# Kernel tuning notes

Hardware: AMD Instinct MI355X
Metric: run time of the kernel (lower is better)

## Reference

```python
import jax, jax.numpy as jnp
import numpy as np


def setup_inputs() -> dict:
    key = jax.random.key(0)
    k1, k2 = jax.random.split(key)
    set1 = jax.random.normal(k1, (8192, 256), dtype=jnp.float32)
    set2 = jax.random.normal(k2, (8192, 256), dtype=jnp.float32)
    return {"set1": set1, "set2": set2}


def reference(set1, set2):
    # Pairwise Euclidean distances via the Gram trick:
    sq1 = jnp.sum(set1 * set1, axis=-1)  # [N]
    sq2 = jnp.sum(set2 * set2, axis=-1)  # [M]
    gram = jnp.einsum('nd,md->nm', set1, set2)  # [N,M]
    d2 = sq1[:, None] + sq2[None, :] - 2.0 * gram
    d = jnp.sqrt(jnp.maximum(d2, 0.0))  # clamp tiny negatives from roundoff
    term_1 = jnp.mean(jnp.min(d, axis=1))  # for each point in set1, nearest in set2
    term_2 = jnp.mean(jnp.min(d, axis=0))  # for each point in set2, nearest in set1
    return term_1 + term_2
```

## Files before the change

### kernel.cpp

```cpp
#include <hip/hip_runtime.h>

#define N_PTS 8192
#define D_DIM 256
#define BN 256
#define BM 256
#define BK 64
#define INF_BITS 0x7F800000u

typedef __attribute__((ext_vector_type(8))) short short8;
typedef __attribute__((ext_vector_type(4))) float f32x4;

__device__ __forceinline__ void gload_lds16(const ushort* g, ushort* l) {
    __builtin_amdgcn_global_load_lds(
        (const __attribute__((address_space(1))) void*)g,
        (__attribute__((address_space(3))) void*)l, 16, 0, 0);
}

__device__ __forceinline__ ushort f2bf(float x) {
    unsigned u = __float_as_uint(x);
    return (ushort)((u + 0x7FFFu + ((u >> 16) & 1u)) >> 16);
}

__global__ void prep_kernel(const float* __restrict__ s1, const float* __restrict__ s2,
                            ushort* __restrict__ b1, ushort* __restrict__ b2,
                            float* __restrict__ sq1, float* __restrict__ sq2,
                            unsigned* __restrict__ rowmin2, unsigned* __restrict__ colmin2) {
    const int half = N_PTS * D_DIM;
    int t = blockIdx.x * 256 + threadIdx.x;
    int e = t * 8;
    bool first = e < half;
    const float* src = first ? s1 : s2;
    ushort* dst = first ? b1 : b2;
    int off = first ? e : e - half;
    float4 v0 = *(const float4*)(src + off);
    float4 v1 = *(const float4*)(src + off + 4);
    float s = v0.x * v0.x + v0.y * v0.y + v0.z * v0.z + v0.w * v0.w
            + v1.x * v1.x + v1.y * v1.y + v1.z * v1.z + v1.w * v1.w;
    ushort4 o0 = { f2bf(v0.x), f2bf(v0.y), f2bf(v0.z), f2bf(v0.w) };
    ushort4 o1 = { f2bf(v1.x), f2bf(v1.y), f2bf(v1.z), f2bf(v1.w) };
    *(ushort4*)(dst + off)     = o0;
    *(ushort4*)(dst + off + 4) = o1;
    #pragma unroll
    for (int m = 1; m <= 16; m <<= 1) s += __shfl_xor(s, m, 64);
    int sub = threadIdx.x & 31;
    int row = off >> 8;
    if (sub == 0) (first ? sq1 : sq2)[row] = s;
    if (sub == 1) (first ? rowmin2 : colmin2)[row] = INF_BITS;
}

__device__ __forceinline__ void stage256(const ushort* __restrict__ g, ushort* l, int tid) {
    #pragma unroll
    for (int r = 0; r < 4; r++) {
        int idx = r * 512 + tid;
        int row = idx >> 3;
        int gc  = (idx & 7) ^ (row & 7);
        gload_lds16(g + (size_t)row * D_DIM + gc * 8, &l[(idx & ~63) * 8]);
    }
}

__global__ __launch_bounds__(512, 2) void tile_kernel(
    const ushort* __restrict__ B1, const ushort* __restrict__ B2,
    const float* __restrict__ sq1, const float* __restrict__ sq2,
    unsigned* __restrict__ rowmin2, unsigned* __restrict__ colmin2) {
    __shared__ ushort As[2][BN * BK] __attribute__((aligned(16)));
    __shared__ ushort Bs[2][BM * BK] __attribute__((aligned(16)));
    __shared__ unsigned rs[BN];
    __shared__ unsigned cs[BM];

    const int tid  = threadIdx.x;
    const int lane = tid & 63;
    const int w    = tid >> 6;
    const int quad = lane >> 4;
    const int c    = lane & 15;
    const int n_off = (w >> 2) * 128;
    const int m_off = (w & 3) * 64;
    const int n0 = blockIdx.y * BN;
    const int m0 = blockIdx.x * BM;

    if (tid < BN) rs[tid] = INF_BITS;
    else          cs[tid - BN] = INF_BITS;

    f32x4 acc[8][4];
    #pragma unroll
    for (int ti = 0; ti < 8; ti++)
        #pragma unroll
        for (int tj = 0; tj < 4; tj++) acc[ti][tj] = (f32x4){0.f, 0.f, 0.f, 0.f};

    const ushort* gA = B1 + (size_t)n0 * D_DIM;
    const ushort* gB = B2 + (size_t)m0 * D_DIM;

    stage256(gA, As[0], tid);
    stage256(gB, Bs[0], tid);
    asm volatile("s_waitcnt vmcnt(0)" ::: "memory");
    __builtin_amdgcn_s_barrier();

    #pragma unroll 4
    for (int t = 0; t < 4; ++t) {
        const ushort* cA = As[t & 1];
        const ushort* cB = Bs[t & 1];
        #pragma unroll
        for (int p = 0; p < 4; ++p) {
            const int kk = p >> 1;
            const int h  = p & 1;
            short8 a[4], b[4];
            #pragma unroll
            for (int i = 0; i < 4; i++) {
                int row = n_off + (h * 4 + i) * 16 + c;
                int ch  = (kk * 4 + quad) ^ (row & 7);
                a[i] = *(const short8*)&cA[row * BK + ch * 8];
            }
            #pragma unroll
            for (int j = 0; j < 4; j++) {
                int row = m_off + j * 16 + c;
                int ch  = (kk * 4 + quad) ^ (row & 7);
                b[j] = *(const short8*)&cB[row * BK + ch * 8];
            }
            if (t < 3 && p == 0) stage256(gA + (t + 1) * BK, As[(t + 1) & 1], tid);
            if (t < 3 && p == 1) stage256(gB + (t + 1) * BK, Bs[(t + 1) & 1], tid);

            __builtin_amdgcn_s_barrier();
            asm volatile("s_waitcnt lgkmcnt(0)" ::: "memory");
            __builtin_amdgcn_s_setprio(1);
            #pragma unroll
            for (int i = 0; i < 4; i++)
                #pragma unroll
                for (int j = 0; j < 4; j++)
                    acc[h * 4 + i][j] = __builtin_amdgcn_mfma_f32_16x16x32_bf16(
                        a[i], b[j], acc[h * 4 + i][j], 0, 0, 0);
            __builtin_amdgcn_s_setprio(0);
            if (p == 3 && t < 3) asm volatile("s_waitcnt vmcnt(0)" ::: "memory");
            __builtin_amdgcn_s_barrier();
        }
    }

    float sqm[4];
    #pragma unroll
    for (int tj = 0; tj < 4; tj++) sqm[tj] = sq2[m0 + m_off + tj * 16 + c];
    float cmin[4];
    #pragma unroll
    for (int tj = 0; tj < 4; tj++) cmin[tj] = __uint_as_float(INF_BITS);

    #pragma unroll
    for (int ti = 0; ti < 8; ti++) {
        float4 sqn = *(const float4*)&sq1[n0 + n_off + ti * 16 + quad * 4];
        float rmin[4] = { __uint_as_float(INF_BITS), __uint_as_float(INF_BITS),
                          __uint_as_float(INF_BITS), __uint_as_float(INF_BITS) };
        #pragma unroll
        for (int tj = 0; tj < 4; tj++) {
            float sn[4] = { sqn.x, sqn.y, sqn.z, sqn.w };
            #pragma unroll
            for (int r = 0; r < 4; r++) {
                float d2 = fmaxf(sn[r] + sqm[tj] - 2.f * acc[ti][tj][r], 0.f);
                rmin[r]  = fminf(rmin[r], d2);
                cmin[tj] = fminf(cmin[tj], d2);
            }
        }
        #pragma unroll
        for (int m = 1; m <= 8; m <<= 1)
            #pragma unroll
            for (int r = 0; r < 4; r++)
                rmin[r] = fminf(rmin[r], __shfl_xor(rmin[r], m, 64));
        if (c == 0) {
            #pragma unroll
            for (int r = 0; r < 4; r++)
                atomicMin(&rs[n_off + ti * 16 + quad * 4 + r], __float_as_uint(rmin[r]));
        }
    }
    #pragma unroll
    for (int m = 16; m <= 32; m <<= 1)
        #pragma unroll
        for (int tj = 0; tj < 4; tj++)
            cmin[tj] = fminf(cmin[tj], __shfl_xor(cmin[tj], m, 64));
    if (quad == 0) {
        #pragma unroll
        for (int tj = 0; tj < 4; tj++)
            atomicMin(&cs[m_off + tj * 16 + c], __float_as_uint(cmin[tj]));
    }
    __syncthreads();

    if (tid < BN) atomicMin(&rowmin2[n0 + tid], rs[tid]);
    else          atomicMin(&colmin2[m0 + tid - BN], cs[tid - BN]);
}

__global__ __launch_bounds__(1024) void reduce_kernel(const unsigned* __restrict__ mins,
                                                      float* __restrict__ out) {
    int tid = threadIdx.x;
    uint4 v[4];
    #pragma unroll
    for (int j = 0; j < 4; j++) v[j] = ((const uint4*)mins)[j * 1024 + tid];
    float s = 0.f;
    #pragma unroll
    for (int j = 0; j < 4; j++)
        s += sqrtf(__uint_as_float(v[j].x)) + sqrtf(__uint_as_float(v[j].y))
           + sqrtf(__uint_as_float(v[j].z)) + sqrtf(__uint_as_float(v[j].w));
    #pragma unroll
    for (int m = 32; m > 0; m >>= 1) s += __shfl_xor(s, m, 64);
    __shared__ float ws[16];
    int lane = tid & 63, wv = tid >> 6;
    if (lane == 0) ws[wv] = s;
    __syncthreads();
    if (tid < 16) {
        float t = ws[tid];
        #pragma unroll
        for (int m = 8; m > 0; m >>= 1) t += __shfl_xor(t, m, 64);
        if (tid == 0) out[0] = t / (float)N_PTS;
    }
}

extern "C" void kernel_launch(void* const* d_in, const int* in_sizes, int n_in,
                              void* d_out, int out_size, void* d_ws, size_t ws_size,
                              hipStream_t stream) {
    const float* set1 = (const float*)d_in[0];
    const float* set2 = (const float*)d_in[1];
    float* out = (float*)d_out;

    unsigned* rowmin2 = (unsigned*)d_ws;
    unsigned* colmin2 = rowmin2 + N_PTS;
    float* sq1 = (float*)(colmin2 + N_PTS);
    float* sq2 = sq1 + N_PTS;
    ushort* b1 = (ushort*)((char*)d_ws + 128 * 1024);
    ushort* b2 = b1 + (size_t)N_PTS * D_DIM;

    prep_kernel<<<(2 * N_PTS * D_DIM) / (256 * 8), 256, 0, stream>>>(
        set1, set2, b1, b2, sq1, sq2, rowmin2, colmin2);
    tile_kernel<<<dim3(N_PTS / BM, N_PTS / BN), 512, 0, stream>>>(
        b1, b2, sq1, sq2, rowmin2, colmin2);
    reduce_kernel<<<1, 1024, 0, stream>>>(rowmin2, out);
}
```

Baseline: 122.3 us.

## Switch to BK=32 triple-buffered LDS pipeline with two-stage prefetch

Result: no change. 120.0 us (-2.0%).

```diff
diff --git a/kernel.cpp b/kernel.cpp
--- a/kernel.cpp
+++ b/kernel.cpp
@@ -4,7 +4,8 @@
 #define D_DIM 256
 #define BN 256
 #define BM 256
-#define BK 64
+#define BK 32
+#define NT (D_DIM / BK)
 #define INF_BITS 0x7F800000u
 
 typedef __attribute__((ext_vector_type(8))) short short8;
@@ -48,13 +49,15 @@
     if (sub == 1) (first ? rowmin2 : colmin2)[row] = INF_BITS;
 }
 
-__device__ __forceinline__ void stage256(const ushort* __restrict__ g, ushort* l, int tid) {
-    #pragma unroll
-    for (int r = 0; r < 4; r++) {
+__device__ __forceinline__ void stage_tile(const ushort* __restrict__ gsrc,
+                                           ushort* ldsbuf, int tid, int kt) {
+    #pragma unroll
+    for (int r = 0; r < 2; r++) {
         int idx = r * 512 + tid;
-        int row = idx >> 3;
-        int gc  = (idx & 7) ^ (row & 7);
-        gload_lds16(g + (size_t)row * D_DIM + gc * 8, &l[(idx & ~63) * 8]);
+        int row = idx >> 2;
+        int gc  = (idx & 3) ^ ((row >> 1) & 3);
+        gload_lds16(gsrc + (size_t)row * D_DIM + kt * BK + gc * 8,
+                    &ldsbuf[(idx & ~63) * 8]);
     }
 }
 
@@ -62,8 +65,8 @@
     const ushort* __restrict__ B1, const ushort* __restrict__ B2,
     const float* __restrict__ sq1, const float* __restrict__ sq2,
     unsigned* __restrict__ rowmin2, unsigned* __restrict__ colmin2) {
-    __shared__ ushort As[2][BN * BK] __attribute__((aligned(16)));
-    __shared__ ushort Bs[2][BM * BK] __attribute__((aligned(16)));
+    __shared__ ushort As[3][BN * BK] __attribute__((aligned(16)));
+    __shared__ ushort Bs[3][BM * BK] __attribute__((aligned(16)));
     __shared__ unsigned rs[BN];
     __shared__ unsigned cs[BM];
 
@@ -89,48 +92,67 @@
     const ushort* gA = B1 + (size_t)n0 * D_DIM;
     const ushort* gB = B2 + (size_t)m0 * D_DIM;
 
-    stage256(gA, As[0], tid);
-    stage256(gB, Bs[0], tid);
-    asm volatile("s_waitcnt vmcnt(0)" ::: "memory");
+    stage_tile(gA, As[0], tid, 0);
+    stage_tile(gB, Bs[0], tid, 0);
+    stage_tile(gA, As[1], tid, 1);
+    stage_tile(gB, Bs[1], tid, 1);
+    asm volatile("s_waitcnt vmcnt(4)" ::: "memory");
     __builtin_amdgcn_s_barrier();
-
-    #pragma unroll 4
-    for (int t = 0; t < 4; ++t) {
-        const ushort* cA = As[t & 1];
-        const ushort* cB = Bs[t & 1];
-        #pragma unroll
-        for (int p = 0; p < 4; ++p) {
-            const int kk = p >> 1;
-            const int h  = p & 1;
-            short8 a[4], b[4];
-            #pragma unroll
-            for (int i = 0; i < 4; i++) {
-                int row = n_off + (h * 4 + i) * 16 + c;
-                int ch  = (kk * 4 + quad) ^ (row & 7);
-                a[i] = *(const short8*)&cA[row * BK + ch * 8];
-            }
-            #pragma unroll
-            for (int j = 0; j < 4; j++) {
-                int row = m_off + j * 16 + c;
-                int ch  = (kk * 4 + quad) ^ (row & 7);
-                b[j] = *(const short8*)&cB[row * BK + ch * 8];
-            }
-            if (t < 3 && p == 0) stage256(gA + (t + 1) * BK, As[(t + 1) & 1], tid);
-            if (t < 3 && p == 1) stage256(gB + (t + 1) * BK, Bs[(t + 1) & 1], tid);
-
-            __builtin_amdgcn_s_barrier();
-            asm volatile("s_waitcnt lgkmcnt(0)" ::: "memory");
-            __builtin_amdgcn_s_setprio(1);
-            #pragma unroll
-            for (int i = 0; i < 4; i++)
-                #pragma unroll
-                for (int j = 0; j < 4; j++)
-                    acc[h * 4 + i][j] = __builtin_amdgcn_mfma_f32_16x16x32_bf16(
-                        a[i], b[j], acc[h * 4 + i][j], 0, 0, 0);
-            __builtin_amdgcn_s_setprio(0);
-            if (p == 3 && t < 3) asm volatile("s_waitcnt vmcnt(0)" ::: "memory");
-            __builtin_amdgcn_s_barrier();
-        }
+    __builtin_amdgcn_sched_barrier(0);
+
+    #pragma unroll
+    for (int t = 0; t < NT; ++t) {
+        const int cur = t % 3;
+        const ushort* cA = As[cur];
+        const ushort* cB = Bs[cur];
+        short8 a[4], b[4];
+        #pragma unroll
+        for (int tj = 0; tj < 4; tj++) {
+            int row = m_off + tj * 16 + c;
+            int ch  = quad ^ ((row >> 1) & 3);
+            b[tj] = *(const short8*)&cB[row * BK + ch * 8];
+        }
+        #pragma unroll
+        for (int ti = 0; ti < 4; ti++) {
+            int row = n_off + ti * 16 + c;
+            int ch  = quad ^ ((row >> 1) & 3);
+            a[ti] = *(const short8*)&cA[row * BK + ch * 8];
+        }
+        if (t + 2 < NT) stage_tile(gA, As[(t + 2) % 3], tid, t + 2);
+        __builtin_amdgcn_s_barrier();
+        __builtin_amdgcn_sched_barrier(0);
+        __builtin_amdgcn_s_setprio(1);
+        #pragma unroll
+        for (int ti = 0; ti < 4; ti++)
+            #pragma unroll
+            for (int tj = 0; tj < 4; tj++)
+                acc[ti][tj] = __builtin_amdgcn_mfma_f32_16x16x32_bf16(
+                    a[ti], b[tj], acc[ti][tj], 0, 0, 0);
+        __builtin_amdgcn_s_setprio(0);
+        __builtin_amdgcn_s_barrier();
+        __builtin_amdgcn_sched_barrier(0);
+        short8 a1[4];
+        #pragma unroll
+        for (int ti = 0; ti < 4; ti++) {
+            int row = n_off + 64 + ti * 16 + c;
+            int ch  = quad ^ ((row >> 1) & 3);
+            a1[ti] = *(const short8*)&cA[row * BK + ch * 8];
+        }
+        if (t + 2 < NT) stage_tile(gB, Bs[(t + 2) % 3], tid, t + 2);
+        __builtin_amdgcn_s_barrier();
+        __builtin_amdgcn_sched_barrier(0);
+        __builtin_amdgcn_s_setprio(1);
+        #pragma unroll
+        for (int ti = 0; ti < 4; ti++)
+            #pragma unroll
+            for (int tj = 0; tj < 4; tj++)
+                acc[4 + ti][tj] = __builtin_amdgcn_mfma_f32_16x16x32_bf16(
+                    a1[ti], b[tj], acc[4 + ti][tj], 0, 0, 0);
+        __builtin_amdgcn_s_setprio(0);
+        if (t < NT - 2)       { asm volatile("s_waitcnt vmcnt(4)" ::: "memory"); }
+        else if (t == NT - 2) { asm volatile("s_waitcnt vmcnt(0)" ::: "memory"); }
+        __builtin_amdgcn_s_barrier();
+        __builtin_amdgcn_sched_barrier(0);
     }
 
     float sqm[4];
```
